# Kernel tuning notes

Measured on AMD Instinct MI355X. Metric: run time of the kernel, lower is better.

Reference implementation:

```python
import jax, jax.numpy as jnp
import numpy as np

N_HEADS = 8
ATT_DIM = 64


def _pos_enc(x):
    # x: (chan, L, bs, D); sinusoidal PE added along axis -3 (the query/key slot dim)
    L, D = x.shape[-3], x.shape[-1]
    pos = np.arange(L)[:, None].astype(np.float32)
    div = np.exp(np.arange(0, D, 2).astype(np.float32) * (-np.log(10000.0) / D))
    pe = np.zeros((L, 1, D), dtype=np.float32)
    pe[:, 0, 0::2] = np.sin(pos * div)
    pe[:, 0, 1::2] = np.cos(pos * div)
    return x + jnp.asarray(pe)


def setup_inputs() -> dict:
    key = jax.random.key(0)
    ks = jax.random.split(key, 6)
    C, NQ, NK, B, QD, KD = 8, 16, 32, 128, 128, 128
    E = N_HEADS * ATT_DIM  # 512
    OUT = ATT_DIM  # out_dim defaults to attention_dim
    b = np.float32(1.0 / np.sqrt(ATT_DIM))
    bp = np.float32(1.0 / np.sqrt(OUT))
    return {
        "q": jax.random.normal(ks[0], (C, NQ, B, QD), dtype=jnp.float32),
        "k": jax.random.normal(ks[1], (C, NK, B, KD), dtype=jnp.float32),
        "Wq": jax.random.uniform(ks[2], (C, NQ, QD, E), jnp.float32, -b, b),
        "Wk": jax.random.uniform(ks[3], (C, NK, KD, E), jnp.float32, -b, b),
        "Wv": jax.random.uniform(ks[4], (C, NK, KD, E), jnp.float32, -b, b),
        "Wp": jax.random.uniform(ks[5], (C, NQ, E, OUT), jnp.float32, -bp, bp),
    }


def reference(q, k, Wq, Wk, Wv, Wp):
    H, A = N_HEADS, ATT_DIM
    C, NQ, B, _ = q.shape
    NK = k.shape[1]
    inv_temp = jnp.float32(1.0 / np.sqrt(A))
    q_pe = _pos_enc(q)
    k_pe = _pos_enc(k)
    # per-channel grouped QKV projections: (C, N, B, D) x (C, N, D, E) -> (C, N, B, E)
    query = jnp.einsum('cqbd,cqde->cqbe', q_pe, Wq).reshape(C, NQ, B, H, A)
    key_t = jnp.einsum('ckbd,ckde->ckbe', k_pe, Wk).reshape(C, NK, B, H, A)
    value = jnp.einsum('ckbd,ckde->ckbe', k_pe, Wv).reshape(C, NK, B, H, A)
    # attention scores per (channel, batch, head)
    logits = jnp.einsum('cqbha,ckbha->cbhqk', query, key_t) * inv_temp
    attn = jax.nn.softmax(logits, axis=-1)
    # value aggregation (original does broadcast-multiply+sum; einsum is the same math)
    out = jnp.einsum('cbhqk,ckbha->cqbha', attn, value).reshape(C, NQ, B, H * A)
    # per-channel output projection
    return jnp.einsum('cqbe,cqeo->cqbo', out, Wp)
```

## Files before the change

kernel.cpp:

```cpp
#include <hip/hip_runtime.h>

#define C_  8
#define NQ_ 16
#define NK_ 32
#define B_  128
#define D_  128
#define E_  512
#define H_  8
#define A_  64
#define O_  64

typedef __attribute__((ext_vector_type(4))) float f32x4;
typedef __attribute__((ext_vector_type(8))) short bf16x8;

__device__ __forceinline__ short f2bf(float f) {
    union { float f; unsigned u; } v; v.f = f;
    unsigned r = v.u + 0x7fffu + ((v.u >> 16) & 1u);
    return (short)(r >> 16);
}

__global__ __launch_bounds__(256) void qkv_proj_kernel(
    const float* __restrict__ qin, const float* __restrict__ kin,
    const float* __restrict__ Wq, const float* __restrict__ Wk,
    const float* __restrict__ Wv,
    short* __restrict__ wsq, short* __restrict__ wsk, short* __restrict__ wsv)
{
    __shared__ __align__(16) short Alds[B_][72];
    __shared__ __align__(16) short Blds[128][72];
    __shared__ float pe_buf[D_];

    const int tid   = threadIdx.x;
    const int blk   = blockIdx.x;
    const int e_blk = blk & 3;
    const int unit  = blk >> 2;

    const float* X; const float* W; short* Y; int n;
    if (unit < C_ * NQ_) {
        n = unit % NQ_;
        X = qin + (size_t)unit * B_ * D_;
        W = Wq  + (size_t)unit * D_ * E_;
        Y = wsq + (size_t)unit * B_ * E_;
    } else if (unit < C_ * (NQ_ + NK_)) {
        const int u = unit - C_ * NQ_;
        n = u % NK_;
        X = kin + (size_t)u * B_ * D_;
        W = Wk  + (size_t)u * D_ * E_;
        Y = wsk + (size_t)u * B_ * E_;
    } else {
        const int u = unit - C_ * (NQ_ + NK_);
        n = u % NK_;
        X = kin + (size_t)u * B_ * D_;
        W = Wv  + (size_t)u * D_ * E_;
        Y = wsv + (size_t)u * B_ * E_;
    }

    if (tid < D_) {
        const int d = tid;
        const float freq = expf((float)(d & ~1) * (-9.210340371976184f / (float)D_));
        const float arg  = (float)n * freq;
        pe_buf[d] = (d & 1) ? cosf(arg) : sinf(arg);
    }
    __syncthreads();

    const int wv   = tid >> 6;
    const int lane = tid & 63;
    const int lr   = lane & 15;
    const int quad = lane >> 4;
    const int wrow = (wv >> 1) * 64;
    const int wcol = (wv & 1) * 64;

    f32x4 acc[4][4];
    for (int m = 0; m < 4; ++m)
        for (int nf = 0; nf < 4; ++nf)
            acc[m][nf] = (f32x4){0.f, 0.f, 0.f, 0.f};

    for (int k0 = 0; k0 < D_; k0 += 64) {
        {
            const int row  = tid >> 1;
            const int kseg = (tid & 1) * 32;
            const float* src = X + (size_t)row * D_ + k0 + kseg;
            for (int i = 0; i < 4; ++i) {
                bf16x8 v;
                for (int j = 0; j < 8; ++j)
                    v[j] = f2bf(src[i * 8 + j] + pe_buf[k0 + kseg + i * 8 + j]);
                *(bf16x8*)&Alds[row][kseg + i * 8] = v;
            }
        }
        {
            const int e  = tid & 127;
            const int kg = (tid >> 7) * 32;
            const float* src = W + (size_t)(k0 + kg) * E_ + e_blk * 128 + e;
            for (int i = 0; i < 4; ++i) {
                bf16x8 v;
                for (int j = 0; j < 8; ++j)
                    v[j] = f2bf(src[(size_t)(i * 8 + j) * E_]);
                *(bf16x8*)&Blds[e][kg + i * 8] = v;
            }
        }
        __syncthreads();

        for (int ks = 0; ks < 2; ++ks) {
            const int kc = ks * 32 + quad * 8;
            bf16x8 af[4], bf[4];
            for (int m = 0; m < 4; ++m)
                af[m] = *(const bf16x8*)&Alds[wrow + m * 16 + lr][kc];
            for (int nf = 0; nf < 4; ++nf)
                bf[nf] = *(const bf16x8*)&Blds[wcol + nf * 16 + lr][kc];
            for (int m = 0; m < 4; ++m)
                for (int nf = 0; nf < 4; ++nf)
                    acc[m][nf] = __builtin_amdgcn_mfma_f32_16x16x32_bf16(
                        af[m], bf[nf], acc[m][nf], 0, 0, 0);
        }
        __syncthreads();
    }

    for (int m = 0; m < 4; ++m)
        for (int nf = 0; nf < 4; ++nf)
            for (int r = 0; r < 4; ++r) {
                const int row = wrow + m * 16 + quad * 4 + r;
                const int col = e_blk * 128 + wcol + nf * 16 + lr;
                Y[(size_t)row * E_ + col] = f2bf(acc[m][nf][r]);
            }
}

__global__ __launch_bounds__(256) void attn_kernel(
    const short* __restrict__ wsq, const short* __restrict__ wsk,
    const short* __restrict__ wsv, short* __restrict__ wso)
{
    __shared__ __align__(16) short Plds[4][16][40];

    const int tid  = threadIdx.x;
    const int wv   = tid >> 6;
    const int lane = tid & 63;
    const int lr   = lane & 15;
    const int quad = lane >> 4;
    const int gw   = blockIdx.x * 4 + wv;
    const int h = gw & (H_ - 1);
    const int b = (gw >> 3) & (B_ - 1);
    const int c = gw >> 10;

    f32x4 sacc[2];
    sacc[0] = (f32x4){0.f, 0.f, 0.f, 0.f};
    sacc[1] = (f32x4){0.f, 0.f, 0.f, 0.f};
    for (int ks = 0; ks < 2; ++ks) {
        const bf16x8 aq = *(const bf16x8*)(wsq +
            ((size_t)(c * NQ_ + lr) * B_ + b) * E_ + h * A_ + ks * 32 + quad * 8);
        for (int t = 0; t < 2; ++t) {
            const bf16x8 bk = *(const bf16x8*)(wsk +
                ((size_t)(c * NK_ + t * 16 + lr) * B_ + b) * E_ + h * A_ + ks * 32 + quad * 8);
            sacc[t] = __builtin_amdgcn_mfma_f32_16x16x32_bf16(aq, bk, sacc[t], 0, 0, 0);
        }
    }

    float p0[4], p1[4];
    for (int r = 0; r < 4; ++r) {
        const float v0 = sacc[0][r] * 0.125f;
        const float v1 = sacc[1][r] * 0.125f;
        float m = fmaxf(v0, v1);
        m = fmaxf(m, __shfl_xor(m, 1));
        m = fmaxf(m, __shfl_xor(m, 2));
        m = fmaxf(m, __shfl_xor(m, 4));
        m = fmaxf(m, __shfl_xor(m, 8));
        const float e0 = __expf(v0 - m);
        const float e1 = __expf(v1 - m);
        float s = e0 + e1;
        s += __shfl_xor(s, 1);
        s += __shfl_xor(s, 2);
        s += __shfl_xor(s, 4);
        s += __shfl_xor(s, 8);
        const float inv = 1.0f / s;
        p0[r] = e0 * inv;
        p1[r] = e1 * inv;
    }

    for (int r = 0; r < 4; ++r) {
        Plds[wv][quad * 4 + r][lr]      = f2bf(p0[r]);
        Plds[wv][quad * 4 + r][16 + lr] = f2bf(p1[r]);
    }
    __syncthreads();
    const bf16x8 ap = *(const bf16x8*)&Plds[wv][lr][quad * 8];

    const size_t vstride = (size_t)B_ * E_;
    const short* vb = wsv + ((size_t)(c * NK_ + quad * 8) * B_ + b) * E_ + h * A_;
    for (int t = 0; t < 4; ++t) {
        bf16x8 bvv;
        for (int j = 0; j < 8; ++j)
            bvv[j] = vb[(size_t)j * vstride + t * 16 + lr];
        f32x4 oacc = (f32x4){0.f, 0.f, 0.f, 0.f};
        oacc = __builtin_amdgcn_mfma_f32_16x16x32_bf16(ap, bvv, oacc, 0, 0, 0);
        for (int r = 0; r < 4; ++r)
            wso[((size_t)(c * NQ_ + quad * 4 + r) * B_ + b) * E_ + h * A_ + t * 16 + lr]
                = f2bf(oacc[r]);
    }
}

__global__ __launch_bounds__(256) void out_proj_kernel(
    const short* __restrict__ wso, const float* __restrict__ Wp,
    float* __restrict__ out)
{
    __shared__ __align__(16) short Xlds[64][72];
    __shared__ __align__(16) short Wlds[64][72];

    const int tid  = threadIdx.x;
    const int blk  = blockIdx.x;
    const int cq   = blk >> 1;
    const int half = blk & 1;

    const short* Xb = wso + (size_t)cq * B_ * E_ + (size_t)half * 64 * E_;
    const float* Wb = Wp  + (size_t)cq * E_ * O_;
    float*       Ob = out + (size_t)cq * B_ * O_ + (size_t)half * 64 * O_;

    const int wv   = tid >> 6;
    const int lane = tid & 63;
    const int lr   = lane & 15;
    const int quad = lane >> 4;

    f32x4 acc[4];
    for (int nf = 0; nf < 4; ++nf) acc[nf] = (f32x4){0.f, 0.f, 0.f, 0.f};

    for (int k0 = 0; k0 < E_; k0 += 64) {
        for (int i = 0; i < 2; ++i) {
            const int task = tid + 256 * i;
            const int row  = task >> 3;
            const int oct  = task & 7;
            *(bf16x8*)&Xlds[row][oct * 8] =
                *(const bf16x8*)(Xb + (size_t)row * E_ + k0 + oct * 8);
        }
        {
            const int o   = tid & 63;
            const int grp = tid >> 6;
            bf16x8 w0, w1;
            for (int j = 0; j < 8; ++j) {
                w0[j] = f2bf(Wb[(size_t)(k0 + grp * 16 + j)     * O_ + o]);
                w1[j] = f2bf(Wb[(size_t)(k0 + grp * 16 + 8 + j) * O_ + o]);
            }
            *(bf16x8*)&Wlds[o][grp * 16]     = w0;
            *(bf16x8*)&Wlds[o][grp * 16 + 8] = w1;
        }
        __syncthreads();

        for (int ks = 0; ks < 2; ++ks) {
            const int kc = ks * 32 + quad * 8;
            const bf16x8 af = *(const bf16x8*)&Xlds[wv * 16 + lr][kc];
            for (int nf = 0; nf < 4; ++nf) {
                const bf16x8 bf = *(const bf16x8*)&Wlds[nf * 16 + lr][kc];
                acc[nf] = __builtin_amdgcn_mfma_f32_16x16x32_bf16(af, bf, acc[nf], 0, 0, 0);
            }
        }
        __syncthreads();
    }

    for (int nf = 0; nf < 4; ++nf)
        for (int r = 0; r < 4; ++r)
            Ob[(size_t)(wv * 16 + quad * 4 + r) * O_ + nf * 16 + lr] = acc[nf][r];
}

extern "C" void kernel_launch(void* const* d_in, const int* in_sizes, int n_in,
                              void* d_out, int out_size, void* d_ws, size_t ws_size,
                              hipStream_t stream) {
    const float* q  = (const float*)d_in[0];
    const float* k  = (const float*)d_in[1];
    const float* Wq = (const float*)d_in[2];
    const float* Wk = (const float*)d_in[3];
    const float* Wv = (const float*)d_in[4];
    const float* Wp = (const float*)d_in[5];
    float* out = (float*)d_out;

    const size_t sz_q = (size_t)C_ * NQ_ * B_ * E_;
    const size_t sz_k = (size_t)C_ * NK_ * B_ * E_;
    short* wsq = (short*)d_ws;
    short* wsk = wsq + sz_q;
    short* wsv = wsk + sz_k;
    short* wso = wsv + sz_k;

    qkv_proj_kernel<<<dim3(2560), dim3(256), 0, stream>>>(q, k, Wq, Wk, Wv, wsq, wsk, wsv);
    attn_kernel<<<dim3(2048), dim3(256), 0, stream>>>(wsq, wsk, wsv, wso);
    out_proj_kernel<<<dim3(256), dim3(256), 0, stream>>>(wso, Wp, out);
}
```

Measured before the change: 265.9 us.

## Stage attention Q/K/V in LDS per block and batch global loads before converts

The attention kernel now uses one block per (channel, batch, half of the heads). It loads the Q, K and V rows for that slice into LDS with coalesced 16-byte loads, instead of each wave doing scattered global gathers, especially the strided per-element V reads. The QKV and output projection kernels now issue all global loads into registers first (vectorized f32x4 loads for the activations) and then convert to bf16 and store to LDS, so more loads are in flight at once. The cost is more LDS and register use per block, and a changed grid mapping in the attention kernel.

```diff
diff --git a/kernel.cpp b/kernel.cpp
--- a/kernel.cpp
+++ b/kernel.cpp
@@ -12,6 +12,7 @@
 
 typedef __attribute__((ext_vector_type(4))) float f32x4;
 typedef __attribute__((ext_vector_type(8))) short bf16x8;
+typedef __attribute__((ext_vector_type(4))) short bf16x4;
 
 __device__ __forceinline__ short f2bf(float f) {
     union { float f; unsigned u; } v; v.f = f;
@@ -74,42 +75,56 @@
         for (int nf = 0; nf < 4; ++nf)
             acc[m][nf] = (f32x4){0.f, 0.f, 0.f, 0.f};
 
+    const int e  = tid & 127;
+    const int kg = (tid >> 7) * 32;
+
     for (int k0 = 0; k0 < D_; k0 += 64) {
-        {
-            const int row  = tid >> 1;
-            const int kseg = (tid & 1) * 32;
-            const float* src = X + (size_t)row * D_ + k0 + kseg;
-            for (int i = 0; i < 4; ++i) {
-                bf16x8 v;
-                for (int j = 0; j < 8; ++j)
-                    v[j] = f2bf(src[i * 8 + j] + pe_buf[k0 + kseg + i * 8 + j]);
-                *(bf16x8*)&Alds[row][kseg + i * 8] = v;
-            }
-        }
-        {
-            const int e  = tid & 127;
-            const int kg = (tid >> 7) * 32;
-            const float* src = W + (size_t)(k0 + kg) * E_ + e_blk * 128 + e;
-            for (int i = 0; i < 4; ++i) {
-                bf16x8 v;
-                for (int j = 0; j < 8; ++j)
-                    v[j] = f2bf(src[(size_t)(i * 8 + j) * E_]);
-                *(bf16x8*)&Blds[e][kg + i * 8] = v;
-            }
+        f32x4 a_raw[8];
+        #pragma unroll
+        for (int i = 0; i < 8; ++i) {
+            const int id  = tid + 256 * i;
+            const int row = id >> 4;
+            const int ch  = id & 15;
+            a_raw[i] = *(const f32x4*)(X + (size_t)row * D_ + k0 + ch * 4);
+        }
+        float b_raw[32];
+        const float* bsrc = W + (size_t)(k0 + kg) * E_ + e_blk * 128 + e;
+        #pragma unroll
+        for (int i = 0; i < 32; ++i)
+            b_raw[i] = bsrc[(size_t)i * E_];
+
+        #pragma unroll
+        for (int i = 0; i < 8; ++i) {
+            const int id  = tid + 256 * i;
+            const int row = id >> 4;
+            const int ch  = id & 15;
+            bf16x4 v;
+            #pragma unroll
+            for (int j = 0; j < 4; ++j)
+                v[j] = f2bf(a_raw[i][j] + pe_buf[k0 + ch * 4 + j]);
+            *(bf16x4*)&Alds[row][ch * 4] = v;
+        }
+        #pragma unroll
+        for (int i = 0; i < 4; ++i) {
+            bf16x8 v;
+            #pragma unroll
+            for (int j = 0; j < 8; ++j)
+                v[j] = f2bf(b_raw[i * 8 + j]);
+            *(bf16x8*)&Blds[e][kg + i * 8] = v;
         }
         __syncthreads();
 
         for (int ks = 0; ks < 2; ++ks) {
             const int kc = ks * 32 + quad * 8;
-            bf16x8 af[4], bf[4];
+            bf16x8 af[4], bfr[4];
             for (int m = 0; m < 4; ++m)
                 af[m] = *(const bf16x8*)&Alds[wrow + m * 16 + lr][kc];
             for (int nf = 0; nf < 4; ++nf)
-                bf[nf] = *(const bf16x8*)&Blds[wcol + nf * 16 + lr][kc];
+                bfr[nf] = *(const bf16x8*)&Blds[wcol + nf * 16 + lr][kc];
             for (int m = 0; m < 4; ++m)
                 for (int nf = 0; nf < 4; ++nf)
                     acc[m][nf] = __builtin_amdgcn_mfma_f32_16x16x32_bf16(
-                        af[m], bf[nf], acc[m][nf], 0, 0, 0);
+                        af[m], bfr[nf], acc[m][nf], 0, 0, 0);
         }
         __syncthreads();
     }
@@ -127,35 +142,69 @@
     const short* __restrict__ wsq, const short* __restrict__ wsk,
     const short* __restrict__ wsv, short* __restrict__ wso)
 {
-    __shared__ __align__(16) short Plds[4][16][40];
-
-    const int tid  = threadIdx.x;
+    __shared__ __align__(16) short Qs[16][264];
+    __shared__ __align__(16) short Ks[32][264];
+    __shared__ __align__(16) short Vs[32][258];
+    __shared__ __align__(16) short Ps[4][16][40];
+
+    const int tid = threadIdx.x;
+    const int blk = blockIdx.x;
+    const int hh  = blk & 1;
+    const int b   = (blk >> 1) & (B_ - 1);
+    const int c   = blk >> 8;
+
+    const size_t rowstride = (size_t)B_ * E_;
+    const size_t ebase = (size_t)b * E_ + hh * 256;
+
+    {
+        const int nloc = tid >> 5;
+        const int bi   = tid & 31;
+        const short* qb = wsq + (size_t)c * NQ_ * rowstride + ebase + bi * 8;
+        const short* kb = wsk + (size_t)c * NK_ * rowstride + ebase + bi * 8;
+        const short* vb = wsv + (size_t)c * NK_ * rowstride + ebase + bi * 8;
+        #pragma unroll
+        for (int i = 0; i < 2; ++i) {
+            const int nn = nloc + i * 8;
+            *(bf16x8*)&Qs[nn][bi * 8] = *(const bf16x8*)(qb + (size_t)nn * rowstride);
+        }
+        #pragma unroll
+        for (int i = 0; i < 4; ++i) {
+            const int nn = nloc + i * 8;
+            *(bf16x8*)&Ks[nn][bi * 8] = *(const bf16x8*)(kb + (size_t)nn * rowstride);
+        }
+        #pragma unroll
+        for (int i = 0; i < 4; ++i) {
+            const int nn = nloc + i * 8;
+            bf16x8 v = *(const bf16x8*)(vb + (size_t)nn * rowstride);
+            #pragma unroll
+            for (int p = 0; p < 4; ++p)
+                *(int*)&Vs[nn][bi * 8 + p * 2] = ((const int*)&v)[p];
+        }
+    }
+    __syncthreads();
+
     const int wv   = tid >> 6;
     const int lane = tid & 63;
     const int lr   = lane & 15;
     const int quad = lane >> 4;
-    const int gw   = blockIdx.x * 4 + wv;
-    const int h = gw & (H_ - 1);
-    const int b = (gw >> 3) & (B_ - 1);
-    const int c = gw >> 10;
-
-    f32x4 sacc[2];
-    sacc[0] = (f32x4){0.f, 0.f, 0.f, 0.f};
-    sacc[1] = (f32x4){0.f, 0.f, 0.f, 0.f};
+    const int lcol = wv * 64;
+
+    f32x4 sacc0 = (f32x4){0.f, 0.f, 0.f, 0.f};
+    f32x4 sacc1 = (f32x4){0.f, 0.f, 0.f, 0.f};
+    #pragma unroll
     for (int ks = 0; ks < 2; ++ks) {
-        const bf16x8 aq = *(const bf16x8*)(wsq +
-            ((size_t)(c * NQ_ + lr) * B_ + b) * E_ + h * A_ + ks * 32 + quad * 8);
-        for (int t = 0; t < 2; ++t) {
-            const bf16x8 bk = *(const bf16x8*)(wsk +
-                ((size_t)(c * NK_ + t * 16 + lr) * B_ + b) * E_ + h * A_ + ks * 32 + quad * 8);
-            sacc[t] = __builtin_amdgcn_mfma_f32_16x16x32_bf16(aq, bk, sacc[t], 0, 0, 0);
-        }
+        const int kc = lcol + ks * 32 + quad * 8;
+        const bf16x8 aq  = *(const bf16x8*)&Qs[lr][kc];
+        const bf16x8 bk0 = *(const bf16x8*)&Ks[lr][kc];
+        const bf16x8 bk1 = *(const bf16x8*)&Ks[16 + lr][kc];
+        sacc0 = __builtin_amdgcn_mfma_f32_16x16x32_bf16(aq, bk0, sacc0, 0, 0, 0);
+        sacc1 = __builtin_amdgcn_mfma_f32_16x16x32_bf16(aq, bk1, sacc1, 0, 0, 0);
     }
 
     float p0[4], p1[4];
     for (int r = 0; r < 4; ++r) {
-        const float v0 = sacc[0][r] * 0.125f;
-        const float v1 = sacc[1][r] * 0.125f;
+        const float v0 = sacc0[r] * 0.125f;
+        const float v1 = sacc1[r] * 0.125f;
         float m = fmaxf(v0, v1);
         m = fmaxf(m, __shfl_xor(m, 1));
         m = fmaxf(m, __shfl_xor(m, 2));
@@ -174,23 +223,23 @@
     }
 
     for (int r = 0; r < 4; ++r) {
-        Plds[wv][quad * 4 + r][lr]      = f2bf(p0[r]);
-        Plds[wv][quad * 4 + r][16 + lr] = f2bf(p1[r]);
+        Ps[wv][quad * 4 + r][lr]      = f2bf(p0[r]);
+        Ps[wv][quad * 4 + r][16 + lr] = f2bf(p1[r]);
     }
     __syncthreads();
-    const bf16x8 ap = *(const bf16x8*)&Plds[wv][lr][quad * 8];
-
-    const size_t vstride = (size_t)B_ * E_;
-    const short* vb = wsv + ((size_t)(c * NK_ + quad * 8) * B_ + b) * E_ + h * A_;
+    const bf16x8 ap = *(const bf16x8*)&Ps[wv][lr][quad * 8];
+
+    #pragma unroll
     for (int t = 0; t < 4; ++t) {
         bf16x8 bvv;
+        #pragma unroll
         for (int j = 0; j < 8; ++j)
-            bvv[j] = vb[(size_t)j * vstride + t * 16 + lr];
+            bvv[j] = Vs[quad * 8 + j][lcol + t * 16 + lr];
         f32x4 oacc = (f32x4){0.f, 0.f, 0.f, 0.f};
         oacc = __builtin_amdgcn_mfma_f32_16x16x32_bf16(ap, bvv, oacc, 0, 0, 0);
         for (int r = 0; r < 4; ++r)
-            wso[((size_t)(c * NQ_ + quad * 4 + r) * B_ + b) * E_ + h * A_ + t * 16 + lr]
-                = f2bf(oacc[r]);
+            wso[((size_t)(c * NQ_ + quad * 4 + r) * B_ + b) * E_
+                + hh * 256 + lcol + t * 16 + lr] = f2bf(oacc[r]);
     }
 }
 
@@ -218,33 +267,43 @@
     f32x4 acc[4];
     for (int nf = 0; nf < 4; ++nf) acc[nf] = (f32x4){0.f, 0.f, 0.f, 0.f};
 
+    const int o   = tid & 63;
+    const int grp = tid >> 6;
+
     for (int k0 = 0; k0 < E_; k0 += 64) {
+        bf16x8 xv[2];
+        #pragma unroll
         for (int i = 0; i < 2; ++i) {
             const int task = tid + 256 * i;
             const int row  = task >> 3;
             const int oct  = task & 7;
-            *(bf16x8*)&Xlds[row][oct * 8] =
-                *(const bf16x8*)(Xb + (size_t)row * E_ + k0 + oct * 8);
-        }
-        {
-            const int o   = tid & 63;
-            const int grp = tid >> 6;
-            bf16x8 w0, w1;
-            for (int j = 0; j < 8; ++j) {
-                w0[j] = f2bf(Wb[(size_t)(k0 + grp * 16 + j)     * O_ + o]);
-                w1[j] = f2bf(Wb[(size_t)(k0 + grp * 16 + 8 + j) * O_ + o]);
-            }
-            *(bf16x8*)&Wlds[o][grp * 16]     = w0;
-            *(bf16x8*)&Wlds[o][grp * 16 + 8] = w1;
-        }
+            xv[i] = *(const bf16x8*)(Xb + (size_t)row * E_ + k0 + oct * 8);
+        }
+        float wr[16];
+        #pragma unroll
+        for (int j = 0; j < 16; ++j)
+            wr[j] = Wb[(size_t)(k0 + grp * 16 + j) * O_ + o];
+
+        #pragma unroll
+        for (int i = 0; i < 2; ++i) {
+            const int task = tid + 256 * i;
+            const int row  = task >> 3;
+            const int oct  = task & 7;
+            *(bf16x8*)&Xlds[row][oct * 8] = xv[i];
+        }
+        bf16x8 w0, w1;
+        #pragma unroll
+        for (int j = 0; j < 8; ++j) { w0[j] = f2bf(wr[j]); w1[j] = f2bf(wr[8 + j]); }
+        *(bf16x8*)&Wlds[o][grp * 16]     = w0;
+        *(bf16x8*)&Wlds[o][grp * 16 + 8] = w1;
         __syncthreads();
 
         for (int ks = 0; ks < 2; ++ks) {
             const int kc = ks * 32 + quad * 8;
             const bf16x8 af = *(const bf16x8*)&Xlds[wv * 16 + lr][kc];
             for (int nf = 0; nf < 4; ++nf) {
-                const bf16x8 bf = *(const bf16x8*)&Wlds[nf * 16 + lr][kc];
-                acc[nf] = __builtin_amdgcn_mfma_f32_16x16x32_bf16(af, bf, acc[nf], 0, 0, 0);
+                const bf16x8 bfr = *(const bf16x8*)&Wlds[nf * 16 + lr][kc];
+                acc[nf] = __builtin_amdgcn_mfma_f32_16x16x32_bf16(af, bfr, acc[nf], 0, 0, 0);
             }
         }
         __syncthreads();
```

After: 248.2 us. -6.7%, faster.
